# Performance work log

Measured on AMD Instinct MI355X. Metric: run time of the kernel, lower is better.

The kernel has to match this reference:

```python
import jax, jax.numpy as jnp
import numpy as np

B, C_IN, FH, TW = 64, 8, 128, 128
FBINS, A, M_ARR, M_SRC = 257, 360, 4, 2
EPS = 1e-6


def _conv2d(x, w):
    return jax.lax.conv_general_dilated(x, w, (1, 1), 'SAME', dimension_numbers=('NCHW', 'OIHW', 'NCHW'))


def _bn(x, g, b, m, v):
    sh = (1, -1, 1, 1)
    return (x - m.reshape(sh)) * jax.lax.rsqrt(v.reshape(sh) + 1e-5) * g.reshape(sh) + b.reshape(sh)


def _pool2(x):
    b_, c, h, w = x.shape
    return x.reshape(b_, c, h // 2, 2, w // 2, 2).max(axis=(3, 5))


def _block(x, w, g, b, m, v):
    return _pool2(jax.nn.relu(_bn(_conv2d(x, w), g, b, m, v)))


def _conv1d(x, w, b):
    return jax.lax.conv_general_dilated(x, w, (1,), 'SAME', dimension_numbers=('NCH', 'OIH', 'NCH')) + b[None, :, None]


def setup_inputs() -> dict:
    ks = jax.random.split(jax.random.key(0), 16)
    r = lambda i, shp, s=1.0: jax.random.normal(ks[i], shp, dtype=jnp.float32) * s
    d = {
        'X': r(0, (B, C_IN, FH, TW)),
        'sv_real': r(1, (B, FBINS, A, M_ARR)),
        'sv_imag': r(2, (B, FBINS, A, M_ARR)),
        'correlation': jnp.zeros((1,), jnp.float32),
        'conv1_w': r(3, (64, C_IN, 3, 3), 0.1),
        'conv2_w': r(4, (64, 64, 3, 3), 0.04),
        'conv3_w': r(5, (64, 64, 3, 3), 0.04),
        'conv4_w': r(6, (FBINS, 64, 3, 3), 0.04),
        'fc_w': r(7, (32, 64), 0.1),
        'fc_b': jnp.zeros((32,), jnp.float32),
        'convs2_w': r(8, (FBINS, FBINS, 3), 0.02),
        'convs2_b': jnp.zeros((FBINS,), jnp.float32),
        'convs1_w': r(9, (1, FBINS, 3), 0.03),
        'convs1_b': jnp.zeros((1,), jnp.float32),
        'ca_w1': r(10, (16, FBINS), 0.06),
        'ca_w2': r(11, (FBINS, 16), 0.2),
    }
    for i, c in [(1, 64), (2, 64), (3, 64), (4, FBINS)]:
        d[f'bn{i}_g'] = jnp.ones((c,), jnp.float32)
        d[f'bn{i}_b'] = jnp.zeros((c,), jnp.float32)
        d[f'bn{i}_m'] = jnp.zeros((c,), jnp.float32)
        d[f'bn{i}_v'] = jnp.ones((c,), jnp.float32)
    return d


def reference(X, sv_real, sv_imag, correlation,
              conv1_w, bn1_g, bn1_b, bn1_m, bn1_v,
              conv2_w, bn2_g, bn2_b, bn2_m, bn2_v,
              conv3_w, bn3_g, bn3_b, bn3_m, bn3_v,
              conv4_w, bn4_g, bn4_b, bn4_m, bn4_v,
              fc_w, fc_b, convs2_w, convs2_b, convs1_w, convs1_b,
              ca_w1, ca_w2):
    b_ = X.shape[0]
    # CNN encoder: (B,8,128,128) -> (B,257,8,8)
    z = _block(X, conv1_w, bn1_g, bn1_b, bn1_m, bn1_v)
    z = _block(z, conv2_w, bn2_g, bn2_b, bn2_m, bn2_v)
    z = _block(z, conv3_w, bn3_g, bn3_b, bn3_m, bn3_v)
    z = _block(z, conv4_w, bn4_g, bn4_b, bn4_m, bn4_v)
    z = z.reshape(b_, FBINS, -1) @ fc_w.T + fc_b            # (B,257,32)
    z = z.reshape(b_, FBINS, C_IN // 2, C_IN)               # (B,257,4,8)
    Rz = jax.lax.complex(z[..., :M_ARR], z[..., M_ARR:])    # (B,257,4,4)
    # hermitianize + diagonal loading
    Rz = 0.5 * (Rz + jnp.conj(jnp.swapaxes(Rz, -1, -2)))
    Rz = Rz + 1e-5 * jnp.eye(M_ARR, dtype=Rz.dtype)
    _, evecs = jnp.linalg.eigh(Rz)                          # ascending eigenvalues
    Un = evecs[..., ::-1][..., M_SRC:]                      # noise subspace (B,F,4,2)
    UnUnH = Un @ jnp.conj(jnp.swapaxes(Un, -1, -2))         # (B,F,4,4)
    svc = jnp.conj(jax.lax.complex(sv_real, sv_imag))       # (B,F,A,4)
    # faithful to torch code: denom[a] = sum_{m,n} conj(sv[a,m]) UnUnH[m,n] conj(sv[a,n])
    denom = jnp.real(jnp.einsum('bfam,bfmn,bfan->bfa', svc, UnUnH, svc))
    spectrum = 1.0 / jnp.maximum(denom, EPS)                # (B,257,360)
    spectrum = jax.nn.leaky_relu(_conv1d(spectrum, convs2_w, convs2_b), 0.1)
    # channel attention over the 257 freq channels
    y = spectrum.mean(-1)                                   # (B,257)
    att = jax.nn.sigmoid(jax.nn.relu(y @ ca_w1.T) @ ca_w2.T)
    spectrum = spectrum * att[:, :, None]
    spectrum = jax.nn.sigmoid(_conv1d(spectrum, convs1_w, convs1_b))[:, 0, :]  # (B,360)
    # soft-argmax over top-5 peaks
    angles = jnp.linspace(0.0, 360.0, A + 1)[:-1]
    vals, idx = jax.lax.top_k(spectrum, 5)
    wts = jax.nn.softmax(20.0 * vals, axis=-1)
    doa = (wts * angles[idx]).sum(-1)[:, None]              # (B,1)
    return doa, spectrum
```

## Files before the change

kernel.cpp:

```cpp
#include <hip/hip_runtime.h>

typedef unsigned short u16;
typedef unsigned int u32;
typedef short short8 __attribute__((ext_vector_type(8)));
typedef float f32x4 __attribute__((ext_vector_type(4)));

#define NB 64
#define NFB 257
#define NANG 360

template<int V> struct IC { static constexpr int value = V; };

__device__ __forceinline__ u16 f2bf(float x) {
    u32 u = __float_as_uint(x);
    u = (u + 0x7fffu + ((u >> 16) & 1u)) >> 16;
    return (u16)u;
}
__device__ __forceinline__ float bf2f(u16 h) { return __uint_as_float(((u32)h) << 16); }


__global__ __launch_bounds__(256) void bnprep(
    const float* g1, const float* b1, const float* m1, const float* v1,
    const float* g2, const float* b2, const float* m2, const float* v2,
    const float* g3, const float* b3, const float* m3, const float* v3,
    const float* g4, const float* b4, const float* m4, const float* v4,
    float* out)
{
    int L = blockIdx.x;
    const float* gs[4] = {g1, g2, g3, g4};
    const float* bs[4] = {b1, b2, b3, b4};
    const float* ms[4] = {m1, m2, m3, m4};
    const float* vs[4] = {v1, v2, v3, v4};
    int n = (L == 3) ? 257 : 64;
    float* sc = out + L * 1024;
    float* bi = sc + 512;
    for (int i = threadIdx.x; i < n; i += 256) {
        float s = gs[L][i] * rsqrtf(vs[L][i] + 1e-5f);
        sc[i] = s;
        bi[i] = bs[L][i] - ms[L][i] * s;
    }
}

__global__ __launch_bounds__(256) void bpack(
    const float* __restrict__ w, u16* __restrict__ Bp,
    int CREAL, int OCREAL, int NT, int KCC, int NFTOT)
{
    int i = blockIdx.x * 256 + threadIdx.x;
    int total = NT * KCC * 2 * NFTOT * 64;
    if (i >= total) return;
    int lane = i & 63;
    int t = i >> 6;
    int nf = t % NFTOT;
    int th = t / NFTOT;
    int h = th & 1;
    int chunk = th >> 1;
    int s = chunk / KCC, kc = chunk % KCC;
    int n = nf * 16 + (lane & 15);
    int k0 = kc * 32 + (lane >> 4) * 8;
    u16 o8[8];
    #pragma unroll
    for (int e = 0; e < 8; ++e) {
        int k = k0 + e;
        float v = 0.f;
        if (k < CREAL && n < OCREAL) v = w[((size_t)n * CREAL + k) * NT + s];
        u16 hh = f2bf(v);
        o8[e] = (h == 0) ? hh : f2bf(v - bf2f(hh));
    }
    u16* d = Bp + (size_t)i * 8;
    #pragma unroll
    for (int e = 0; e < 8; ++e) d[e] = o8[e];
}

__global__ __launch_bounds__(256) void bpack1(const float* __restrict__ w, u16* __restrict__ Bp)
{
    int i = blockIdx.x * 256 + threadIdx.x;
    if (i >= 3 * 2 * 4 * 64) return;
    int lane = i & 63;
    int t = i >> 6;
    int nf = t % 4;
    int th = t / 4;
    int h = th & 1;
    int ky = th >> 1;
    int n = nf * 16 + (lane & 15);
    int q = lane >> 4;
    u16 o8[8];
    #pragma unroll
    for (int e = 0; e < 8; ++e) {
        float v = (q < 3) ? w[((size_t)(n * 8 + e) * 3 + ky) * 3 + q] : 0.f;
        u16 hh = f2bf(v);
        o8[e] = (h == 0) ? hh : f2bf(v - bf2f(hh));
    }
    u16* d = Bp + (size_t)i * 8;
    #pragma unroll
    for (int e = 0; e < 8; ++e) d[e] = o8[e];
}

__global__ __launch_bounds__(256) void xpack_kernel(
    const float* __restrict__ X, u16* __restrict__ xp)
{
    __shared__ float Xs[8][132];
    int bid = blockIdx.x;
    int prow = bid % 130;
    int b = bid / 130;
    bool inr = (prow >= 1 && prow <= 128);
    for (int i = threadIdx.x; i < 8 * 130; i += 256) {
        int c = i / 130, pcol = i % 130;
        float v = 0.f;
        if (inr && pcol >= 1 && pcol <= 128)
            v = X[(((size_t)b * 8 + c) * 128 + (prow - 1)) * 128 + (pcol - 1)];
        Xs[c][pcol] = v;
    }
    __syncthreads();
    for (int p = threadIdx.x; p < 130; p += 256) {
        short8 h8, l8;
        #pragma unroll
        for (int c = 0; c < 8; ++c) {
            float f = Xs[c][p];
            u16 hh = f2bf(f);
            h8[c] = (short)hh;
            l8[c] = (short)f2bf(f - bf2f(hh));
        }
        size_t o = (((size_t)b * 130 + prow) * 130 + p) * 16;
        *(short8*)(xp + o) = h8;
        *(short8*)(xp + o + 8) = l8;
    }
}

__global__ __launch_bounds__(256) void zpad(
    u32* buf, int Bn, int Hp, int Wp, int wpp, int doCols)
{
    int perB = 2 * Wp + (doCols ? 2 * (Hp - 2) : 0);
    long total = (long)Bn * perB * wpp;
    for (long idx = blockIdx.x * 256L + threadIdx.x; idx < total; idx += (long)gridDim.x * 256) {
        int w = (int)(idx % wpp);
        long t = idx / wpp;
        int p = (int)(t % perB);
        int b = (int)(t / perB);
        int row, col;
        if (p < Wp) { row = 0; col = p; }
        else if (p < 2 * Wp) { row = Hp - 1; col = p - Wp; }
        else { int pp = p - 2 * Wp; row = 1 + (pp >> 1); col = (pp & 1) ? (Wp - 1) : 0; }
        buf[(((size_t)b * Hp + row) * Wp + col) * (size_t)wpp + w] = 0;
    }
}

__global__ __launch_bounds__(256) void conv_c1(
    const u16* __restrict__ A, const u16* __restrict__ Bp,
    const float* __restrict__ esc, const float* __restrict__ ebi,
    u16* __restrict__ O)
{
    constexpr int Wst = 130, Hp = 130;
    constexpr int SROWS = 5;
    constexpr int SPIX = SROWS * Wst;
    __shared__ __align__(16) char sm[SPIX * 48];

    int bid = blockIdx.x;
    int ytile = bid % 64;
    int b = bid / 64;
    int y0 = ytile * 2;
    int tid = threadIdx.x;
    int wv = tid >> 6;
    int l = tid & 63;
    int r = l & 15, q = l >> 4;

    #pragma unroll
    for (int it = 0; it < 3; ++it) {
        int pix = tid + it * 256;
        int prow = y0 + pix / Wst, pcol = pix % Wst;
        uint4 v0 = {0, 0, 0, 0}, v1 = {0, 0, 0, 0};
        if (pix < SPIX && prow < Hp) {
            const u16* src = A + (((size_t)b * Hp + prow) * Wst + pcol) * 16;
            v0 = *(const uint4*)src;
            v1 = *(const uint4*)(src + 8);
        }
        if (pix < SPIX) {
            *(uint4*)(sm + pix * 48) = v0;
            *(uint4*)(sm + pix * 48 + 16) = v1;
        }
    }
    __syncthreads();

    f32x4 acc[4][4] = {};

    #pragma unroll
    for (int ky = 0; ky < 3; ++ky) {
        short8 bh[4], bl[4];
        #pragma unroll
        for (int ni = 0; ni < 4; ++ni) {
            const u16* bt = Bp + ((size_t)(ky * 2) * 4 + ni) * 512 + l * 8;
            bh[ni] = *(const short8*)bt;
            bl[ni] = *(const short8*)(bt + 4 * 512);
        }
        short8 ah[4], al[4];
        #pragma unroll
        for (int mi = 0; mi < 4; ++mi) {
            int pf = wv * 2 + (mi >> 1);
            int y = mi & 1;
            int p = (y + ky) * Wst + pf * 16 + r + q;
            ah[mi] = *(const short8*)(sm + p * 48);
            al[mi] = *(const short8*)(sm + p * 48 + 16);
        }
        #pragma unroll
        for (int ni = 0; ni < 4; ++ni)
            #pragma unroll
            for (int mi = 0; mi < 4; ++mi)
                acc[mi][ni] = __builtin_amdgcn_mfma_f32_16x16x32_bf16(ah[mi], bh[ni], acc[mi][ni], 0, 0, 0);
        #pragma unroll
        for (int ni = 0; ni < 4; ++ni)
            #pragma unroll
            for (int mi = 0; mi < 4; ++mi)
                acc[mi][ni] = __builtin_amdgcn_mfma_f32_16x16x32_bf16(ah[mi], bl[ni], acc[mi][ni], 0, 0, 0);
        #pragma unroll
        for (int ni = 0; ni < 4; ++ni)
            #pragma unroll
            for (int mi = 0; mi < 4; ++mi)
                acc[mi][ni] = __builtin_amdgcn_mfma_f32_16x16x32_bf16(al[mi], bh[ni], acc[mi][ni], 0, 0, 0);
    }

    #pragma unroll
    for (int ni = 0; ni < 4; ++ni) {
        int oc = ni * 16 + r;
        float sc0 = esc[oc], bi0 = ebi[oc];
        #pragma unroll
        for (int pi = 0; pi < 2; ++pi) {
            int pf = wv * 2 + pi;
            #pragma unroll
            for (int k = 0; k < 2; ++k) {
                float m = -3.4e38f;
                #pragma unroll
                for (int dmi = 0; dmi < 2; ++dmi)
                    #pragma unroll
                    for (int dj = 0; dj < 2; ++dj)
                        m = fmaxf(m, fmaf(acc[2 * pi + dmi][ni][2 * k + dj], sc0, bi0));
                m = fmaxf(m, 0.f);
                int x2 = pf * 8 + q * 2 + k;
                size_t base = (((size_t)b * 66 + (y0 / 2 + 1)) * 66 + (x2 + 1)) * 128;
                u16* d = O + base + ((oc >> 5) << 6) + (oc & 31);
                u16 hh = f2bf(m);
                d[0] = hh;
                d[32] = f2bf(m - bf2f(hh));
            }
        }
    }
}

template<int H, int W, int OC, int R, int NF, int MFW, int OUTMODE, int NFTOT>
__global__ __launch_bounds__(256) void conv_gemm(
    const u16* __restrict__ A, const u16* __restrict__ Bp,
    const float* __restrict__ esc, const float* __restrict__ ebi,
    u16* __restrict__ O, float* __restrict__ Of)
{
    constexpr int Wst = W + 2, Hp = H + 2;
    constexpr int SROWS = R + 2;
    constexpr int SPIX = SROWS * Wst;
    constexpr int XF = W / 16;
    constexpr int HT = H / R;
    constexpr int GR = SPIX * 4;
    constexpr int ROUNDS = (GR + 255) / 256;
    __shared__ __align__(16) char sm[SPIX * 128];

    int bid = blockIdx.x;
    int ytile = bid % HT;
    int b = bid / HT;
    int tid = threadIdx.x;
    int wv = tid >> 6;
    int l = tid & 63;
    int r = l & 15, q = l >> 4;
    int y0 = ytile * R;
    int nfg0 = blockIdx.y * NF;

    f32x4 acc[MFW][NF] = {};
    short8 Bh[2][NF], Bl[2][NF];

    auto loadB = [&](int buf, int chunk) {
        #pragma unroll
        for (int ni = 0; ni < NF; ++ni) {
            const u16* bt = Bp + ((size_t)(chunk * 2) * NFTOT + nfg0 + ni) * 512 + l * 8;
            Bh[buf][ni] = *(const short8*)bt;
            Bl[buf][ni] = *(const short8*)(bt + (size_t)NFTOT * 512);
        }
    };

    #pragma unroll
    for (int it = 0; it < ROUNDS; ++it) {
        int idx = tid + it * 256;
        int pix = idx >> 2, sub = idx & 3;
        int prow = y0 + pix / Wst, pcol = pix % Wst;
        uint4 v0 = {0, 0, 0, 0}, v1 = {0, 0, 0, 0};
        if (idx < GR && prow < Hp) {
            const u16* src = A + (((size_t)b * Hp + prow) * Wst + pcol) * 128 + sub * 8;
            v0 = *(const uint4*)src;
            v1 = *(const uint4*)(src + 32);
        }
        if (idx < GR) {
            *(uint4*)(sm + pix * 128 + ((sub ^ (pix & 7)) << 4)) = v0;
            *(uint4*)(sm + pix * 128 + (((sub + 4) ^ (pix & 7)) << 4)) = v1;
        }
    }
    loadB(0, 0);
    __syncthreads();

    auto computePhase = [&](auto csc) {
        constexpr int cs = decltype(csc)::value;
        #pragma unroll
        for (int s = 0; s < 9; ++s) {
            int cur = (cs * 9 + s) & 1;
            if (s < 8) loadB(cur ^ 1, (s + 1) * 2 + cs);
            else if (cs == 0) loadB(cur ^ 1, 1);
            int ky = s / 3, kx = s % 3;
            short8 ah[MFW], al[MFW];
            #pragma unroll
            for (int mi = 0; mi < MFW; ++mi) {
                int pf = wv * (MFW / 2) + (mi >> 1);
                int y = (pf / XF) * 2 + (mi & 1);
                int xf = pf % XF;
                int p = (y + ky) * Wst + xf * 16 + kx + r;
                int off = p * 128 + ((q ^ (p & 7)) << 4);
                ah[mi] = *(const short8*)(sm + off);
                al[mi] = *(const short8*)(sm + (off ^ 64));
            }
            #pragma unroll
            for (int ni = 0; ni < NF; ++ni)
                #pragma unroll
                for (int mi = 0; mi < MFW; ++mi)
                    acc[mi][ni] = __builtin_amdgcn_mfma_f32_16x16x32_bf16(ah[mi], Bh[cur][ni], acc[mi][ni], 0, 0, 0);
            #pragma unroll
            for (int ni = 0; ni < NF; ++ni)
                #pragma unroll
                for (int mi = 0; mi < MFW; ++mi)
                    acc[mi][ni] = __builtin_amdgcn_mfma_f32_16x16x32_bf16(ah[mi], Bl[cur][ni], acc[mi][ni], 0, 0, 0);
            #pragma unroll
            for (int ni = 0; ni < NF; ++ni)
                #pragma unroll
                for (int mi = 0; mi < MFW; ++mi)
                    acc[mi][ni] = __builtin_amdgcn_mfma_f32_16x16x32_bf16(al[mi], Bh[cur][ni], acc[mi][ni], 0, 0, 0);
        }
    };

    uint4 r0[ROUNDS], r1[ROUNDS];
    #pragma unroll
    for (int it = 0; it < ROUNDS; ++it) {
        int idx = tid + it * 256;
        int pix = idx >> 2, sub = idx & 3;
        int prow = y0 + pix / Wst, pcol = pix % Wst;
        r0[it] = (uint4){0, 0, 0, 0};
        r1[it] = (uint4){0, 0, 0, 0};
        if (idx < GR && prow < Hp) {
            const u16* src = A + (((size_t)b * Hp + prow) * Wst + pcol) * 128 + 64 + sub * 8;
            r0[it] = *(const uint4*)src;
            r1[it] = *(const uint4*)(src + 32);
        }
    }
    computePhase(IC<0>{});
    __syncthreads();
    #pragma unroll
    for (int it = 0; it < ROUNDS; ++it) {
        int idx = tid + it * 256;
        int pix = idx >> 2, sub = idx & 3;
        if (idx < GR) {
            *(uint4*)(sm + pix * 128 + ((sub ^ (pix & 7)) << 4)) = r0[it];
            *(uint4*)(sm + pix * 128 + (((sub + 4) ^ (pix & 7)) << 4)) = r1[it];
        }
    }
    __syncthreads();
    computePhase(IC<1>{});

    #pragma unroll
    for (int ni = 0; ni < NF; ++ni) {
        int oc = (nfg0 + ni) * 16 + r;
        float sc0 = esc[oc], bi0 = ebi[oc];
        #pragma unroll
        for (int pi = 0; pi < MFW / 2; ++pi) {
            int pf = wv * (MFW / 2) + pi;
            int y2 = y0 / 2 + pf / XF;
            int xb = (pf % XF) * 8 + q * 2;
            #pragma unroll
            for (int k = 0; k < 2; ++k) {
                float m = -3.4e38f;
                #pragma unroll
                for (int dmi = 0; dmi < 2; ++dmi)
                    #pragma unroll
                    for (int dj = 0; dj < 2; ++dj)
                        m = fmaxf(m, fmaf(acc[2 * pi + dmi][ni][2 * k + dj], sc0, bi0));
                m = fmaxf(m, 0.f);
                int x2 = xb + k;
                if (OUTMODE == 0) {
                    size_t base = (((size_t)b * (H / 2 + 2) + y2 + 1) * (W / 2 + 2) + (x2 + 1)) * 128;
                    u16* d = O + base + ((oc >> 5) << 6) + (oc & 31);
                    u16 hh = f2bf(m);
                    d[0] = hh;
                    d[32] = f2bf(m - bf2f(hh));
                } else {
                    if (oc < OC)
                        Of[(((size_t)b * (H / 2) + y2) * (W / 2) + x2) * (size_t)OC + oc] = m;
                }
            }
        }
    }
}

__global__ __launch_bounds__(256) void convs2_gemm(
    const u16* __restrict__ A, const u16* __restrict__ Bp,
    const float* __restrict__ bia, float* __restrict__ sp2,
    float* __restrict__ part)
{
    constexpr int SPIX = 194;
    constexpr int GR = SPIX * 4;
    constexpr int ROUNDS = 4;
    __shared__ __align__(16) char sm[SPIX * 128];

    int bid = blockIdx.x;
    int tt = bid & 1;
    int b = bid >> 1;
    int nt = blockIdx.y;
    int t0 = tt * 192;
    int tid = threadIdx.x;
    int wv = tid >> 6;
    int l = tid & 63;
    int r = l & 15, q = l >> 4;

    f32x4 acc[3][3] = {};
    short8 Bh[2][3], Bl[2][3];

    auto loadB = [&](int buf, int chunk) {
        #pragma unroll
        for (int ni = 0; ni < 3; ++ni) {
            const u16* bt = Bp + ((size_t)(chunk * 2) * 18 + nt * 3 + ni) * 512 + l * 8;
            Bh[buf][ni] = *(const short8*)bt;
            Bl[buf][ni] = *(const short8*)(bt + 18 * 512);
        }
    };
    uint4 g0[ROUNDS], g1[ROUNDS];

    auto stageIssue = [&](int cs) {
        #pragma unroll
        for (int it = 0; it < ROUNDS; ++it) {
            int idx = tid + it * 256;
            int pix = idx >> 2, sub = idx & 3;
            int gp = t0 + pix;
            g0[it] = (uint4){0, 0, 0, 0};
            g1[it] = (uint4){0, 0, 0, 0};
            if (idx < GR && gp < 362) {
                const u16* src = A + ((size_t)b * 362 + gp) * 576 + cs * 64 + sub * 8;
                g0[it] = *(const uint4*)src;
                g1[it] = *(const uint4*)(src + 32);
            }
        }
    };
    auto stageWrite = [&]() {
        #pragma unroll
        for (int it = 0; it < ROUNDS; ++it) {
            int idx = tid + it * 256;
            int pix = idx >> 2, sub = idx & 3;
            if (idx < GR) {
                *(uint4*)(sm + pix * 128 + ((sub ^ (pix & 7)) << 4)) = g0[it];
                *(uint4*)(sm + pix * 128 + (((sub + 4) ^ (pix & 7)) << 4)) = g1[it];
            }
        }
    };

    stageIssue(0);
    stageWrite();
    loadB(0, 0);
    __syncthreads();

    #pragma unroll
    for (int cs = 0; cs < 9; ++cs) {
        if (cs < 8) stageIssue(cs + 1);
        #pragma unroll
        for (int ky = 0; ky < 3; ++ky) {
            int cur = (cs * 3 + ky) & 1;
            if (ky < 2) loadB(cur ^ 1, (ky + 1) * 9 + cs);
            else if (cs < 8) loadB(cur ^ 1, cs + 1);
            #pragma unroll
            for (int mi = 0; mi < 3; ++mi) {
                int p = (wv * 3 + mi) * 16 + r + ky;
                int off = p * 128 + ((q ^ (p & 7)) << 4);
                short8 ah = *(const short8*)(sm + off);
                short8 al = *(const short8*)(sm + (off ^ 64));
                #pragma unroll
                for (int ni = 0; ni < 3; ++ni)
                    acc[mi][ni] = __builtin_amdgcn_mfma_f32_16x16x32_bf16(ah, Bh[cur][ni], acc[mi][ni], 0, 0, 0);
                #pragma unroll
                for (int ni = 0; ni < 3; ++ni)
                    acc[mi][ni] = __builtin_amdgcn_mfma_f32_16x16x32_bf16(ah, Bl[cur][ni], acc[mi][ni], 0, 0, 0);
                #pragma unroll
                for (int ni = 0; ni < 3; ++ni)
                    acc[mi][ni] = __builtin_amdgcn_mfma_f32_16x16x32_bf16(al, Bh[cur][ni], acc[mi][ni], 0, 0, 0);
            }
        }
        __syncthreads();
        if (cs < 8) {
            stageWrite();
            __syncthreads();
        }
    }

    float psum[3] = {0.f, 0.f, 0.f};
    #pragma unroll
    for (int ni = 0; ni < 3; ++ni) {
        int n = (nt * 3 + ni) * 16 + r;
        if (n >= NFB) continue;
        float bi0 = bia[n];
        #pragma unroll
        for (int mi = 0; mi < 3; ++mi) {
            int tb = t0 + (wv * 3 + mi) * 16 + q * 4;
            #pragma unroll
            for (int j = 0; j < 4; ++j) {
                int t = tb + j;
                if (t < NANG) {
                    float v = acc[mi][ni][j] + bi0;
                    v = (v >= 0.f) ? v : 0.1f * v;
                    sp2[((size_t)b * NANG + t) * NFB + n] = v;
                    psum[ni] += v;
                }
            }
        }
    }
    float* wred = (float*)sm;
    #pragma unroll
    for (int ni = 0; ni < 3; ++ni) {
        float s = psum[ni];
        s += __shfl_down(s, 32, 64);
        s += __shfl_down(s, 16, 64);
        if (q == 0) wred[(wv * 3 + ni) * 16 + r] = s;
    }
    __syncthreads();
    if (tid < 48) {
        int ni = tid / 16, rr = tid % 16;
        float tot = wred[(0 * 3 + ni) * 16 + rr] + wred[(1 * 3 + ni) * 16 + rr]
                  + wred[(2 * 3 + ni) * 16 + rr] + wred[(3 * 3 + ni) * 16 + rr];
        int n = (nt * 3 + ni) * 16 + rr;
        if (n < NFB) part[((size_t)b * 2 + tt) * NFB + n] = tot;
    }
}

__global__ __launch_bounds__(256) void fc_kernel(
    const float* __restrict__ z, const float* __restrict__ fw,
    const float* __restrict__ fb, float* __restrict__ zfc)
{
    int bid = blockIdx.x;
    int ftile = bid % 33;
    int b = bid / 33;
    int j = threadIdx.x & 31;
    int f = ftile * 8 + (threadIdx.x >> 5);
    if (f >= 257) return;
    const float* zb = z + (size_t)b * 16448;
    float a = fb[j];
    #pragma unroll 8
    for (int s = 0; s < 64; ++s) a = fmaf(zb[s * 257 + f], fw[j * 64 + s], a);
    zfc[((size_t)b * 257 + f) * 32 + j] = a;
}

__global__ __launch_bounds__(64) void eigh_kernel(const float* __restrict__ z, double* __restrict__ rp)
{
    int idx = blockIdx.x * 64 + threadIdx.x;
    if (idx >= NB * NFB) return;
    const float* zr = z + (size_t)idx * 32;
    double Ar[4][4], Ai[4][4], Vr[4][4], Vi[4][4];
    #pragma unroll
    for (int m = 0; m < 4; ++m)
        #pragma unroll
        for (int n = 0; n < 4; ++n) {
            Ar[m][n] = 0.5 * ((double)zr[m * 8 + n] + (double)zr[n * 8 + m]);
            Ai[m][n] = 0.5 * ((double)zr[m * 8 + n + 4] - (double)zr[n * 8 + m + 4]);
            Vr[m][n] = (m == n) ? 1.0 : 0.0;
            Vi[m][n] = 0.0;
        }
    #pragma unroll
    for (int m = 0; m < 4; ++m) Ar[m][m] += 1e-5;

    for (int sweep = 0; sweep < 8; ++sweep) {
        #pragma unroll
        for (int p = 0; p < 3; ++p)
            #pragma unroll
            for (int qq = p + 1; qq < 4; ++qq) {
                double apr = Ar[p][qq], api = Ai[p][qq];
                double rmod = sqrt(apr * apr + api * api);
                if (rmod < 1e-300) continue;
                double cph = apr / rmod, sph = api / rmod;
                double tau = (Ar[qq][qq] - Ar[p][p]) / (2.0 * rmod);
                double t = (tau >= 0.0) ? (-1.0 / (tau + sqrt(1.0 + tau * tau)))
                                        : (1.0 / (-tau + sqrt(1.0 + tau * tau)));
                double c = 1.0 / sqrt(1.0 + t * t);
                double s = t * c;
                double wr = s * cph, wi = s * sph;
                #pragma unroll
                for (int i = 0; i < 4; ++i) {
                    double xr = Ar[i][p], xi = Ai[i][p];
                    double yr = Ar[i][qq], yi = Ai[i][qq];
                    Ar[i][p] = c * xr + (wr * yr + wi * yi);
                    Ai[i][p] = c * xi + (wr * yi - wi * yr);
                    Ar[i][qq] = c * yr - (wr * xr - wi * xi);
                    Ai[i][qq] = c * yi - (wr * xi + wi * xr);
                }
                #pragma unroll
                for (int i = 0; i < 4; ++i) {
                    double xr = Ar[p][i], xi = Ai[p][i];
                    double yr = Ar[qq][i], yi = Ai[qq][i];
                    Ar[p][i] = c * xr + (wr * yr - wi * yi);
                    Ai[p][i] = c * xi + (wr * yi + wi * yr);
                    Ar[qq][i] = c * yr - (wr * xr + wi * xi);
                    Ai[qq][i] = c * yi - (wr * xi - wi * xr);
                }
                #pragma unroll
                for (int i = 0; i < 4; ++i) {
                    double xr = Vr[i][p], xi = Vi[i][p];
                    double yr = Vr[i][qq], yi = Vi[i][qq];
                    Vr[i][p] = c * xr + (wr * yr + wi * yi);
                    Vi[i][p] = c * xi + (wr * yi - wi * yr);
                    Vr[i][qq] = c * yr - (wr * xr - wi * xi);
                    Vi[i][qq] = c * yi - (wr * xi + wi * xr);
                }
            }
    }
    double ev[4] = {Ar[0][0], Ar[1][1], Ar[2][2], Ar[3][3]};
    int i0 = 0;
    #pragma unroll
    for (int k = 1; k < 4; ++k) if (ev[k] < ev[i0]) i0 = k;
    int i1 = (i0 == 0) ? 1 : 0;
    #pragma unroll
    for (int k = 0; k < 4; ++k) if (k != i0 && ev[k] < ev[i1]) i1 = k;
    double* o = rp + (size_t)idx * 16;
    #pragma unroll
    for (int m = 0; m < 4; ++m)
        #pragma unroll
        for (int n = 0; n < 4; ++n)
            o[m * 4 + n] = Vr[m][i0] * Vr[n][i0] + Vi[m][i0] * Vi[n][i0]
                         + Vr[m][i1] * Vr[n][i1] + Vi[m][i1] * Vi[n][i1];
}

__global__ __launch_bounds__(256) void music_kernel(
    const float4* __restrict__ svr, const float4* __restrict__ svi,
    const double* __restrict__ rp, u16* __restrict__ mu)
{
    __shared__ double P[32][16];
    __shared__ float T[32][33];
    int bid = blockIdx.x;
    int at = bid % 12; bid /= 12;
    int ft = bid % 9;
    int b = bid / 9;
    int f0 = ft * 32, a0 = at * 32;
    int tid = threadIdx.x;
    for (int i = tid; i < 32 * 16; i += 256) {
        int fi = i >> 4, j = i & 15;
        int f = f0 + fi;
        P[fi][j] = (f < 257) ? rp[((size_t)b * 257 + f) * 16 + j] : 0.0;
    }
    __syncthreads();
    int asub = tid & 31, fsub = tid >> 5;
    int a = a0 + asub;
    #pragma unroll
    for (int k2 = 0; k2 < 4; ++k2) {
        int fl = fsub + 8 * k2;
        int f = f0 + fl;
        float val = 0.f;
        if (a < 360 && f < 257) {
            float4 u = svr[((size_t)b * 257 + f) * 360 + a];
            float4 w = svi[((size_t)b * 257 + f) * 360 + a];
            const double* Pf = P[fl];
            double ua[4] = {u.x, u.y, u.z, u.w};
            double wa[4] = {w.x, w.y, w.z, w.w};
            double qa = 0.0, qb = 0.0;
            #pragma unroll
            for (int m = 0; m < 4; ++m)
                #pragma unroll
                for (int n = 0; n < 4; ++n) {
                    double pmn = Pf[m * 4 + n];
                    qa += pmn * ua[m] * ua[n];
                    qb += pmn * wa[m] * wa[n];
                }
            double den = qa - qb;
            val = (float)(1.0 / fmax(den, 1e-6));
        }
        T[asub][fl] = val;
    }
    __syncthreads();
    int sec0 = f0 >> 5;
    #pragma unroll
    for (int p = 0; p < 4; ++p) {
        int row = p * 8 + (tid >> 5);
        int fc = tid & 31;
        int a2 = a0 + row;
        if (a2 < 360) {
            float v = T[row][fc];
            u16* d = mu + ((size_t)b * 362 + a2 + 1) * 576 + (size_t)sec0 * 64 + fc;
            u16 hh = f2bf(v);
            d[0] = hh;
            d[32] = f2bf(v - bf2f(hh));
        }
    }
}

__global__ __launch_bounds__(256) void attn_finish(
    const float* __restrict__ part, const float* __restrict__ w1,
    const float* __restrict__ w2, float* __restrict__ att)
{
    __shared__ float ys[257];
    __shared__ float hs[16];
    int b = blockIdx.x;
    int tid = threadIdx.x;
    for (int f = tid; f < 257; f += 256) {
        float s = part[((size_t)b * 2 + 0) * 257 + f] + part[((size_t)b * 2 + 1) * 257 + f];
        ys[f] = s * (1.0f / 360.0f);
    }
    __syncthreads();
    if (tid < 16) {
        float h = 0.f;
        for (int c = 0; c < 257; ++c) h = fmaf(ys[c], w1[(size_t)tid * 257 + c], h);
        hs[tid] = fmaxf(h, 0.f);
    }
    __syncthreads();
    for (int o = tid; o < 257; o += 256) {
        float a = 0.f;
        #pragma unroll
        for (int j = 0; j < 16; ++j) a = fmaf(hs[j], w2[(size_t)o * 16 + j], a);
        att[(size_t)b * 257 + o] = 1.0f / (1.0f + expf(-a));
    }
}

__global__ __launch_bounds__(256) void convs1_kernel(
    const float* __restrict__ sp2, const float* __restrict__ att,
    const float* __restrict__ w, const float* __restrict__ bb,
    float* __restrict__ outS)
{
    int bid = blockIdx.x;
    int tt = bid % 90;
    int b = bid / 90;
    int wv = threadIdx.x >> 6, l = threadIdx.x & 63;
    int t = tt * 4 + wv;
    float s = 0.f;
    for (int f = l; f < 257; f += 64) {
        float av = att[(size_t)b * 257 + f];
        float w0 = w[f * 3] * av, w1 = w[f * 3 + 1] * av, w2 = w[f * 3 + 2] * av;
        const float* col = sp2 + (size_t)b * 360 * 257 + f;
        if (t > 0)   s = fmaf(w0, col[(size_t)(t - 1) * 257], s);
        s = fmaf(w1, col[(size_t)t * 257], s);
        if (t < 359) s = fmaf(w2, col[(size_t)(t + 1) * 257], s);
    }
    #pragma unroll
    for (int off = 32; off > 0; off >>= 1) s += __shfl_down(s, off, 64);
    if (l == 0) outS[(size_t)b * 360 + t] = 1.0f / (1.0f + expf(-(s + bb[0])));
}

__global__ __launch_bounds__(64) void doa_kernel(const float* __restrict__ spec, float* __restrict__ doa)
{
    int b = blockIdx.x;
    int l = threadIdx.x;
    const float* s = spec + (size_t)b * NANG;
    float v[6];
    #pragma unroll
    for (int j = 0; j < 6; ++j) {
        int idx = l + 64 * j;
        v[j] = (idx < NANG) ? s[idx] : -3.4e38f;
    }
    float wvv[5]; int wii[5];
    #pragma unroll
    for (int k = 0; k < 5; ++k) {
        float bv = v[0]; int bj = 0;
        #pragma unroll
        for (int j = 1; j < 6; ++j)
            if (v[j] > bv) { bv = v[j]; bj = j; }
        int bi = l + 64 * bj;
        #pragma unroll
        for (int off = 1; off < 64; off <<= 1) {
            float ov = __shfl_xor(bv, off, 64);
            int oi = __shfl_xor(bi, off, 64);
            if (ov > bv || (ov == bv && oi < bi)) { bv = ov; bi = oi; }
        }
        wvv[k] = bv; wii[k] = bi;
        if ((bi & 63) == l) {
            int j = bi >> 6;
            #pragma unroll
            for (int jj = 0; jj < 6; ++jj)
                if (jj == j) v[jj] = -3.4e38f;
        }
    }
    if (l == 0) {
        float m = wvv[0];
        float wsum = 0.f, asum = 0.f;
        #pragma unroll
        for (int k = 0; k < 5; ++k) {
            float e = expf(20.0f * (wvv[k] - m));
            wsum += e;
            asum += e * (float)wii[k];
        }
        doa[b] = asum / wsum;
    }
}

extern "C" void kernel_launch(void* const* d_in, const int* in_sizes, int n_in,
                              void* d_out, int out_size, void* d_ws, size_t ws_size,
                              hipStream_t stream)
{
    const float* X    = (const float*)d_in[0];
    const float* svr  = (const float*)d_in[1];
    const float* svi  = (const float*)d_in[2];
    const float* c1w  = (const float*)d_in[4];
    const float* c2w  = (const float*)d_in[5];
    const float* c3w  = (const float*)d_in[6];
    const float* c4w  = (const float*)d_in[7];
    const float* fcw  = (const float*)d_in[8];
    const float* fcb  = (const float*)d_in[9];
    const float* s2w  = (const float*)d_in[10];
    const float* s2b  = (const float*)d_in[11];
    const float* s1w  = (const float*)d_in[12];
    const float* s1b  = (const float*)d_in[13];
    const float* caw1 = (const float*)d_in[14];
    const float* caw2 = (const float*)d_in[15];
    const float* bn1g = (const float*)d_in[16]; const float* bn1b = (const float*)d_in[17];
    const float* bn1m = (const float*)d_in[18]; const float* bn1v = (const float*)d_in[19];
    const float* bn2g = (const float*)d_in[20]; const float* bn2b = (const float*)d_in[21];
    const float* bn2m = (const float*)d_in[22]; const float* bn2v = (const float*)d_in[23];
    const float* bn3g = (const float*)d_in[24]; const float* bn3b = (const float*)d_in[25];
    const float* bn3m = (const float*)d_in[26]; const float* bn3v = (const float*)d_in[27];
    const float* bn4g = (const float*)d_in[28]; const float* bn4b = (const float*)d_in[29];
    const float* bn4m = (const float*)d_in[30]; const float* bn4v = (const float*)d_in[31];

    char* wsb = (char*)d_ws;
    u16* xp = (u16*)(wsb + 0);
    u16* c3 = (u16*)(wsb + 0);
    u16* mu = (u16*)(wsb + 0);
    const size_t Bb = 34611200;
    u16*   c2  = (u16*)(wsb + Bb);
    float*  zbuf = (float*)(wsb + Bb);
    float*  zfc  = (float*)(wsb + Bb + 4210688);
    double* rp   = (double*)(wsb + Bb + 6316032);
    float*  sp2  = (float*)(wsb + Bb + 8421376);
    float*  part = (float*)(wsb + Bb + 32106496);
    float*  att  = (float*)(wsb + Bb + 32501248);
    const size_t Cb = Bb + 71368704;
    u16* c4  = (u16*)(wsb + Cb);
    u16* bp1 = (u16*)(wsb + Cb + 5308416);
    u16* bp2 = (u16*)(wsb + Cb + 5382144);
    u16* bp3 = (u16*)(wsb + Cb + 5529600);
    u16* bp4 = (u16*)(wsb + Cb + 5677056);
    u16* bp5 = (u16*)(wsb + Cb + 6414336);
    float* bns = (float*)(wsb + Cb + 7409664);

    float* outD = (float*)d_out;
    float* outS = (float*)d_out + 64;

    bnprep<<<4, 256, 0, stream>>>(bn1g, bn1b, bn1m, bn1v, bn2g, bn2b, bn2m, bn2v,
                                  bn3g, bn3b, bn3m, bn3v, bn4g, bn4b, bn4m, bn4v, bns);
    bpack1<<<6, 256, 0, stream>>>(c1w, bp1);
    bpack<<<36, 256, 0, stream>>>(c2w, bp2, 64, 64, 9, 2, 4);
    bpack<<<36, 256, 0, stream>>>(c3w, bp3, 64, 64, 9, 2, 4);
    bpack<<<180, 256, 0, stream>>>(c4w, bp4, 64, 257, 9, 2, 20);
    bpack<<<243, 256, 0, stream>>>(s2w, bp5, 257, 257, 3, 9, 18);
    xpack_kernel<<<64 * 130, 256, 0, stream>>>(X, xp);
    zpad<<<4160, 256, 0, stream>>>((u32*)c2, 64, 66, 66, 64, 1);
    zpad<<<1088, 256, 0, stream>>>((u32*)c4, 64, 18, 18, 64, 1);

    conv_c1<<<64 * 64, 256, 0, stream>>>(xp, bp1, bns, bns + 512, c2);
    zpad<<<2112, 256, 0, stream>>>((u32*)c3, 64, 34, 34, 64, 1);
    conv_gemm<64, 64, 64, 2, 4, 2, 0, 4>
        <<<dim3(64 * 32, 1), 256, 0, stream>>>(c2, bp2, bns + 1024, bns + 1536, c3, nullptr);
    conv_gemm<32, 32, 64, 4, 4, 2, 0, 4>
        <<<dim3(64 * 8, 1), 256, 0, stream>>>(c3, bp3, bns + 2048, bns + 2560, c4, nullptr);
    zpad<<<144, 256, 0, stream>>>((u32*)mu, 64, 362, 1, 288, 0);
    conv_gemm<16, 16, 257, 8, 4, 2, 1, 20>
        <<<dim3(64 * 2, 5), 256, 0, stream>>>(c4, bp4, bns + 3072, bns + 3584, nullptr, zbuf);

    fc_kernel<<<64 * 33, 256, 0, stream>>>(zbuf, fcw, fcb, zfc);
    eigh_kernel<<<NFB, 64, 0, stream>>>(zfc, rp);
    music_kernel<<<64 * 108, 256, 0, stream>>>((const float4*)svr, (const float4*)svi, rp, mu);
    convs2_gemm<<<dim3(64 * 2, 6), 256, 0, stream>>>(mu, bp5, s2b, sp2, part);

    attn_finish<<<64, 256, 0, stream>>>(part, caw1, caw2, att);
    convs1_kernel<<<64 * 90, 256, 0, stream>>>(sp2, att, s1w, s1b, outS);
    doa_kernel<<<64, 64, 0, stream>>>(outS, outD);
}
```

Before: 416.5 us.

## Merge prep kernels, drop register prefetch staging, retile convs2 into three tiles

Fuses the BN prep, the five weight-pack kernels and the input packer into one prep_kernel, and merges two zero-pad launches into one, to cut launch count. Conv_gemm and convs2_gemm drop their register-held prefetch of the next channel slice and instead load straight to shared memory after a barrier. This lowers register pressure but stops overlapping global loads with MFMA work. Convs2 now splits the 360 angles into three 128-wide tiles instead of two 192-wide ones, which raises block count and shrinks the per-wave accumulators. The attention partial-sum reduction is updated to read three partials.

Result: faster. 395.0 us (-5.2%).

```diff
diff --git a/kernel.cpp b/kernel.cpp
--- a/kernel.cpp
+++ b/kernel.cpp
@@ -19,33 +19,10 @@
 __device__ __forceinline__ float bf2f(u16 h) { return __uint_as_float(((u32)h) << 16); }
 
 
-__global__ __launch_bounds__(256) void bnprep(
-    const float* g1, const float* b1, const float* m1, const float* v1,
-    const float* g2, const float* b2, const float* m2, const float* v2,
-    const float* g3, const float* b3, const float* m3, const float* v3,
-    const float* g4, const float* b4, const float* m4, const float* v4,
-    float* out)
-{
-    int L = blockIdx.x;
-    const float* gs[4] = {g1, g2, g3, g4};
-    const float* bs[4] = {b1, b2, b3, b4};
-    const float* ms[4] = {m1, m2, m3, m4};
-    const float* vs[4] = {v1, v2, v3, v4};
-    int n = (L == 3) ? 257 : 64;
-    float* sc = out + L * 1024;
-    float* bi = sc + 512;
-    for (int i = threadIdx.x; i < n; i += 256) {
-        float s = gs[L][i] * rsqrtf(vs[L][i] + 1e-5f);
-        sc[i] = s;
-        bi[i] = bs[L][i] - ms[L][i] * s;
-    }
-}
-
-__global__ __launch_bounds__(256) void bpack(
+__device__ __forceinline__ void bpack_body(
     const float* __restrict__ w, u16* __restrict__ Bp,
-    int CREAL, int OCREAL, int NT, int KCC, int NFTOT)
-{
-    int i = blockIdx.x * 256 + threadIdx.x;
+    int CREAL, int OCREAL, int NT, int KCC, int NFTOT, int i)
+{
     int total = NT * KCC * 2 * NFTOT * 64;
     if (i >= total) return;
     int lane = i & 63;
@@ -71,59 +48,107 @@
     for (int e = 0; e < 8; ++e) d[e] = o8[e];
 }
 
-__global__ __launch_bounds__(256) void bpack1(const float* __restrict__ w, u16* __restrict__ Bp)
-{
-    int i = blockIdx.x * 256 + threadIdx.x;
-    if (i >= 3 * 2 * 4 * 64) return;
-    int lane = i & 63;
-    int t = i >> 6;
-    int nf = t % 4;
-    int th = t / 4;
-    int h = th & 1;
-    int ky = th >> 1;
-    int n = nf * 16 + (lane & 15);
-    int q = lane >> 4;
-    u16 o8[8];
-    #pragma unroll
-    for (int e = 0; e < 8; ++e) {
-        float v = (q < 3) ? w[((size_t)(n * 8 + e) * 3 + ky) * 3 + q] : 0.f;
-        u16 hh = f2bf(v);
-        o8[e] = (h == 0) ? hh : f2bf(v - bf2f(hh));
-    }
-    u16* d = Bp + (size_t)i * 8;
-    #pragma unroll
-    for (int e = 0; e < 8; ++e) d[e] = o8[e];
-}
-
-__global__ __launch_bounds__(256) void xpack_kernel(
-    const float* __restrict__ X, u16* __restrict__ xp)
+__global__ __launch_bounds__(256) void prep_kernel(
+    const float* __restrict__ X, u16* __restrict__ xp,
+    const float* __restrict__ c1w, u16* __restrict__ bp1,
+    const float* __restrict__ c2w, u16* __restrict__ bp2,
+    const float* __restrict__ c3w, u16* __restrict__ bp3,
+    const float* __restrict__ c4w, u16* __restrict__ bp4,
+    const float* __restrict__ s2w, u16* __restrict__ bp5,
+    const float* g1, const float* b1, const float* m1, const float* v1,
+    const float* g2, const float* b2, const float* m2, const float* v2,
+    const float* g3, const float* b3, const float* m3, const float* v3,
+    const float* g4, const float* b4, const float* m4, const float* v4,
+    float* __restrict__ bns)
 {
     __shared__ float Xs[8][132];
-    int bid = blockIdx.x;
-    int prow = bid % 130;
-    int b = bid / 130;
-    bool inr = (prow >= 1 && prow <= 128);
-    for (int i = threadIdx.x; i < 8 * 130; i += 256) {
-        int c = i / 130, pcol = i % 130;
-        float v = 0.f;
-        if (inr && pcol >= 1 && pcol <= 128)
-            v = X[(((size_t)b * 8 + c) * 128 + (prow - 1)) * 128 + (pcol - 1)];
-        Xs[c][pcol] = v;
-    }
-    __syncthreads();
-    for (int p = threadIdx.x; p < 130; p += 256) {
-        short8 h8, l8;
-        #pragma unroll
-        for (int c = 0; c < 8; ++c) {
-            float f = Xs[c][p];
-            u16 hh = f2bf(f);
-            h8[c] = (short)hh;
-            l8[c] = (short)f2bf(f - bf2f(hh));
-        }
-        size_t o = (((size_t)b * 130 + prow) * 130 + p) * 16;
-        *(short8*)(xp + o) = h8;
-        *(short8*)(xp + o + 8) = l8;
-    }
+    int blk = blockIdx.x;
+    int tid = threadIdx.x;
+    if (blk < 4) {
+        int L = blk;
+        const float* gs[4] = {g1, g2, g3, g4};
+        const float* bs[4] = {b1, b2, b3, b4};
+        const float* ms[4] = {m1, m2, m3, m4};
+        const float* vs[4] = {v1, v2, v3, v4};
+        int n = (L == 3) ? 257 : 64;
+        float* sc = bns + L * 1024;
+        float* bi = sc + 512;
+        for (int i = tid; i < n; i += 256) {
+            float s = gs[L][i] * rsqrtf(vs[L][i] + 1e-5f);
+            sc[i] = s;
+            bi[i] = bs[L][i] - ms[L][i] * s;
+        }
+    } else if (blk < 10) {
+        int i = (blk - 4) * 256 + tid;
+        if (i < 3 * 2 * 4 * 64) {
+            int lane = i & 63;
+            int t = i >> 6;
+            int nf = t % 4;
+            int th = t / 4;
+            int h = th & 1;
+            int ky = th >> 1;
+            int n = nf * 16 + (lane & 15);
+            int q = lane >> 4;
+            u16 o8[8];
+            #pragma unroll
+            for (int e = 0; e < 8; ++e) {
+                float v = (q < 3) ? c1w[((size_t)(n * 8 + e) * 3 + ky) * 3 + q] : 0.f;
+                u16 hh = f2bf(v);
+                o8[e] = (h == 0) ? hh : f2bf(v - bf2f(hh));
+            }
+            u16* d = bp1 + (size_t)i * 8;
+            #pragma unroll
+            for (int e = 0; e < 8; ++e) d[e] = o8[e];
+        }
+    } else if (blk < 46) {
+        bpack_body(c2w, bp2, 64, 64, 9, 2, 4, (blk - 10) * 256 + tid);
+    } else if (blk < 82) {
+        bpack_body(c3w, bp3, 64, 64, 9, 2, 4, (blk - 46) * 256 + tid);
+    } else if (blk < 262) {
+        bpack_body(c4w, bp4, 64, 257, 9, 2, 20, (blk - 82) * 256 + tid);
+    } else if (blk < 505) {
+        bpack_body(s2w, bp5, 257, 257, 3, 9, 18, (blk - 262) * 256 + tid);
+    } else {
+        int row = blk - 505;
+        int prow = row % 130;
+        int b = row / 130;
+        bool inr = (prow >= 1 && prow <= 128);
+        for (int i = tid; i < 8 * 130; i += 256) {
+            int c = i / 130, pcol = i % 130;
+            float v = 0.f;
+            if (inr && pcol >= 1 && pcol <= 128)
+                v = X[(((size_t)b * 8 + c) * 128 + (prow - 1)) * 128 + (pcol - 1)];
+            Xs[c][pcol] = v;
+        }
+        __syncthreads();
+        for (int p = tid; p < 130; p += 256) {
+            short8 h8, l8;
+            #pragma unroll
+            for (int c = 0; c < 8; ++c) {
+                float f = Xs[c][p];
+                u16 hh = f2bf(f);
+                h8[c] = (short)hh;
+                l8[c] = (short)f2bf(f - bf2f(hh));
+            }
+            size_t o = (((size_t)b * 130 + prow) * 130 + p) * 16;
+            *(short8*)(xp + o) = h8;
+            *(short8*)(xp + o + 8) = l8;
+        }
+    }
+}
+
+__device__ __forceinline__ void zpad_body(u32* buf, int Hp, int Wp, int wpp, int doCols, long idx)
+{
+    int perB = 2 * Wp + (doCols ? 2 * (Hp - 2) : 0);
+    int w = (int)(idx % wpp);
+    long t = idx / wpp;
+    int p = (int)(t % perB);
+    int b = (int)(t / perB);
+    int row, col;
+    if (p < Wp) { row = 0; col = p; }
+    else if (p < 2 * Wp) { row = Hp - 1; col = p - Wp; }
+    else { int pp = p - 2 * Wp; row = 1 + (pp >> 1); col = (pp & 1) ? (Wp - 1) : 0; }
+    buf[(((size_t)b * Hp + row) * Wp + col) * (size_t)wpp + w] = 0;
 }
 
 __global__ __launch_bounds__(256) void zpad(
@@ -131,16 +156,17 @@
 {
     int perB = 2 * Wp + (doCols ? 2 * (Hp - 2) : 0);
     long total = (long)Bn * perB * wpp;
-    for (long idx = blockIdx.x * 256L + threadIdx.x; idx < total; idx += (long)gridDim.x * 256) {
-        int w = (int)(idx % wpp);
-        long t = idx / wpp;
-        int p = (int)(t % perB);
-        int b = (int)(t / perB);
-        int row, col;
-        if (p < Wp) { row = 0; col = p; }
-        else if (p < 2 * Wp) { row = Hp - 1; col = p - Wp; }
-        else { int pp = p - 2 * Wp; row = 1 + (pp >> 1); col = (pp & 1) ? (Wp - 1) : 0; }
-        buf[(((size_t)b * Hp + row) * Wp + col) * (size_t)wpp + w] = 0;
+    for (long idx = blockIdx.x * 256L + threadIdx.x; idx < total; idx += (long)gridDim.x * 256)
+        zpad_body(buf, Hp, Wp, wpp, doCols, idx);
+}
+
+__global__ __launch_bounds__(256) void zpad_init(u32* c2b, u32* c4b)
+{
+    const long T1 = 64L * 260 * 64;
+    const long T2 = 64L * 68 * 64;
+    for (long idx = blockIdx.x * 256L + threadIdx.x; idx < T1 + T2; idx += (long)gridDim.x * 256) {
+        if (idx < T1) zpad_body(c2b, 66, 66, 64, 1, idx);
+        else          zpad_body(c4b, 18, 18, 64, 1, idx - T1);
     }
 }
 
@@ -281,24 +307,24 @@
         }
     };
 
-    #pragma unroll
-    for (int it = 0; it < ROUNDS; ++it) {
-        int idx = tid + it * 256;
-        int pix = idx >> 2, sub = idx & 3;
-        int prow = y0 + pix / Wst, pcol = pix % Wst;
-        uint4 v0 = {0, 0, 0, 0}, v1 = {0, 0, 0, 0};
-        if (idx < GR && prow < Hp) {
-            const u16* src = A + (((size_t)b * Hp + prow) * Wst + pcol) * 128 + sub * 8;
-            v0 = *(const uint4*)src;
-            v1 = *(const uint4*)(src + 32);
-        }
-        if (idx < GR) {
-            *(uint4*)(sm + pix * 128 + ((sub ^ (pix & 7)) << 4)) = v0;
-            *(uint4*)(sm + pix * 128 + (((sub + 4) ^ (pix & 7)) << 4)) = v1;
-        }
-    }
-    loadB(0, 0);
-    __syncthreads();
+    auto stage = [&](int cs) {
+        #pragma unroll
+        for (int it = 0; it < ROUNDS; ++it) {
+            int idx = tid + it * 256;
+            int pix = idx >> 2, sub = idx & 3;
+            int prow = y0 + pix / Wst, pcol = pix % Wst;
+            uint4 v0 = {0, 0, 0, 0}, v1 = {0, 0, 0, 0};
+            if (idx < GR && prow < Hp) {
+                const u16* src = A + (((size_t)b * Hp + prow) * Wst + pcol) * 128 + cs * 64 + sub * 8;
+                v0 = *(const uint4*)src;
+                v1 = *(const uint4*)(src + 32);
+            }
+            if (idx < GR) {
+                *(uint4*)(sm + pix * 128 + ((sub ^ (pix & 7)) << 4)) = v0;
+                *(uint4*)(sm + pix * 128 + (((sub + 4) ^ (pix & 7)) << 4)) = v1;
+            }
+        }
+    };
 
     auto computePhase = [&](auto csc) {
         constexpr int cs = decltype(csc)::value;
@@ -337,31 +363,12 @@
         }
     };
 
-    uint4 r0[ROUNDS], r1[ROUNDS];
-    #pragma unroll
-    for (int it = 0; it < ROUNDS; ++it) {
-        int idx = tid + it * 256;
-        int pix = idx >> 2, sub = idx & 3;
-        int prow = y0 + pix / Wst, pcol = pix % Wst;
-        r0[it] = (uint4){0, 0, 0, 0};
-        r1[it] = (uint4){0, 0, 0, 0};
-        if (idx < GR && prow < Hp) {
-            const u16* src = A + (((size_t)b * Hp + prow) * Wst + pcol) * 128 + 64 + sub * 8;
-            r0[it] = *(const uint4*)src;
-            r1[it] = *(const uint4*)(src + 32);
-        }
-    }
+    stage(0);
+    loadB(0, 0);
+    __syncthreads();
     computePhase(IC<0>{});
     __syncthreads();
-    #pragma unroll
-    for (int it = 0; it < ROUNDS; ++it) {
-        int idx = tid + it * 256;
-        int pix = idx >> 2, sub = idx & 3;
-        if (idx < GR) {
-            *(uint4*)(sm + pix * 128 + ((sub ^ (pix & 7)) << 4)) = r0[it];
-            *(uint4*)(sm + pix * 128 + (((sub + 4) ^ (pix & 7)) << 4)) = r1[it];
-        }
-    }
+    stage(1);
     __syncthreads();
     computePhase(IC<1>{});
 
@@ -404,22 +411,21 @@
     const float* __restrict__ bia, float* __restrict__ sp2,
     float* __restrict__ part)
 {
-    constexpr int SPIX = 194;
+    constexpr int SPIX = 130;
     constexpr int GR = SPIX * 4;
-    constexpr int ROUNDS = 4;
     __shared__ __align__(16) char sm[SPIX * 128];
 
     int bid = blockIdx.x;
-    int tt = bid & 1;
-    int b = bid >> 1;
+    int tt = bid % 3;
+    int b = bid / 3;
     int nt = blockIdx.y;
-    int t0 = tt * 192;
+    int t0 = tt * 128;
     int tid = threadIdx.x;
     int wv = tid >> 6;
     int l = tid & 63;
     int r = l & 15, q = l >> 4;
 
-    f32x4 acc[3][3] = {};
+    f32x4 acc[2][3] = {};
     short8 Bh[2][3], Bl[2][3];
 
     auto loadB = [&](int buf, int chunk) {
@@ -430,68 +436,64 @@
             Bl[buf][ni] = *(const short8*)(bt + 18 * 512);
         }
     };
-    uint4 g0[ROUNDS], g1[ROUNDS];
-
-    auto stageIssue = [&](int cs) {
-        #pragma unroll
-        for (int it = 0; it < ROUNDS; ++it) {
+
+    auto stage = [&](int cs) {
+        #pragma unroll
+        for (int it = 0; it < 3; ++it) {
             int idx = tid + it * 256;
             int pix = idx >> 2, sub = idx & 3;
             int gp = t0 + pix;
-            g0[it] = (uint4){0, 0, 0, 0};
-            g1[it] = (uint4){0, 0, 0, 0};
+            uint4 v0 = {0, 0, 0, 0}, v1 = {0, 0, 0, 0};
             if (idx < GR && gp < 362) {
                 const u16* src = A + ((size_t)b * 362 + gp) * 576 + cs * 64 + sub * 8;
-                g0[it] = *(const uint4*)src;
-                g1[it] = *(const uint4*)(src + 32);
+                v0 = *(const uint4*)src;
+                v1 = *(const uint4*)(src + 32);
+            }
+            if (idx < GR) {
+                *(uint4*)(sm + pix * 128 + ((sub ^ (pix & 7)) << 4)) = v0;
+                *(uint4*)(sm + pix * 128 + (((sub + 4) ^ (pix & 7)) << 4)) = v1;
             }
         }
     };
-    auto stageWrite = [&]() {
-        #pragma unroll
-        for (int it = 0; it < ROUNDS; ++it) {
-            int idx = tid + it * 256;
-            int pix = idx >> 2, sub = idx & 3;
-            if (idx < GR) {
-                *(uint4*)(sm + pix * 128 + ((sub ^ (pix & 7)) << 4)) = g0[it];
-                *(uint4*)(sm + pix * 128 + (((sub + 4) ^ (pix & 7)) << 4)) = g1[it];
-            }
-        }
-    };
-
-    stageIssue(0);
-    stageWrite();
+
+    stage(0);
     loadB(0, 0);
     __syncthreads();
 
     #pragma unroll
     for (int cs = 0; cs < 9; ++cs) {
-        if (cs < 8) stageIssue(cs + 1);
         #pragma unroll
         for (int ky = 0; ky < 3; ++ky) {
             int cur = (cs * 3 + ky) & 1;
             if (ky < 2) loadB(cur ^ 1, (ky + 1) * 9 + cs);
             else if (cs < 8) loadB(cur ^ 1, cs + 1);
-            #pragma unroll
-            for (int mi = 0; mi < 3; ++mi) {
-                int p = (wv * 3 + mi) * 16 + r + ky;
+            short8 ah[2], al[2];
+            #pragma unroll
+            for (int mi = 0; mi < 2; ++mi) {
+                int p = (wv * 2 + mi) * 16 + r + ky;
                 int off = p * 128 + ((q ^ (p & 7)) << 4);
-                short8 ah = *(const short8*)(sm + off);
-                short8 al = *(const short8*)(sm + (off ^ 64));
-                #pragma unroll
-                for (int ni = 0; ni < 3; ++ni)
-                    acc[mi][ni] = __builtin_amdgcn_mfma_f32_16x16x32_bf16(ah, Bh[cur][ni], acc[mi][ni], 0, 0, 0);
-                #pragma unroll
-                for (int ni = 0; ni < 3; ++ni)
-                    acc[mi][ni] = __builtin_amdgcn_mfma_f32_16x16x32_bf16(ah, Bl[cur][ni], acc[mi][ni], 0, 0, 0);
-                #pragma unroll
-                for (int ni = 0; ni < 3; ++ni)
-                    acc[mi][ni] = __builtin_amdgcn_mfma_f32_16x16x32_bf16(al, Bh[cur][ni], acc[mi][ni], 0, 0, 0);
-            }
+                ah[mi] = *(const short8*)(sm + off);
+                al[mi] = *(const short8*)(sm + (off ^ 64));
+            }
+            #pragma unroll
+            for (int ni = 0; ni < 3; ++ni)
+                #pragma unroll
+                for (int mi = 0; mi < 2; ++mi)
+                    acc[mi][ni] = __builtin_amdgcn_mfma_f32_16x16x32_bf16(ah[mi], Bh[cur][ni], acc[mi][ni], 0, 0, 0);
+            #pragma unroll
+            for (int ni = 0; ni < 3; ++ni)
+                #pragma unroll
+                for (int mi = 0; mi < 2; ++mi)
+                    acc[mi][ni] = __builtin_amdgcn_mfma_f32_16x16x32_bf16(ah[mi], Bl[cur][ni], acc[mi][ni], 0, 0, 0);
+            #pragma unroll
+            for (int ni = 0; ni < 3; ++ni)
+                #pragma unroll
+                for (int mi = 0; mi < 2; ++mi)
+                    acc[mi][ni] = __builtin_amdgcn_mfma_f32_16x16x32_bf16(al[mi], Bh[cur][ni], acc[mi][ni], 0, 0, 0);
         }
         __syncthreads();
         if (cs < 8) {
-            stageWrite();
+            stage(cs + 1);
             __syncthreads();
         }
     }
@@ -503,8 +505,8 @@
         if (n >= NFB) continue;
         float bi0 = bia[n];
         #pragma unroll
-        for (int mi = 0; mi < 3; ++mi) {
-            int tb = t0 + (wv * 3 + mi) * 16 + q * 4;
+        for (int mi = 0; mi < 2; ++mi) {
+            int tb = t0 + (wv * 2 + mi) * 16 + q * 4;
             #pragma unroll
             for (int j = 0; j < 4; ++j) {
                 int t = tb + j;
@@ -531,7 +533,7 @@
         float tot = wred[(0 * 3 + ni) * 16 + rr] + wred[(1 * 3 + ni) * 16 + rr]
                   + wred[(2 * 3 + ni) * 16 + rr] + wred[(3 * 3 + ni) * 16 + rr];
         int n = (nt * 3 + ni) * 16 + rr;
-        if (n < NFB) part[((size_t)b * 2 + tt) * NFB + n] = tot;
+        if (n < NFB) part[((size_t)b * 3 + tt) * NFB + n] = tot;
     }
 }
 
@@ -701,7 +703,9 @@
     int b = blockIdx.x;
     int tid = threadIdx.x;
     for (int f = tid; f < 257; f += 256) {
-        float s = part[((size_t)b * 2 + 0) * 257 + f] + part[((size_t)b * 2 + 1) * 257 + f];
+        float s = part[((size_t)b * 3 + 0) * 257 + f]
+                + part[((size_t)b * 3 + 1) * 257 + f]
+                + part[((size_t)b * 3 + 2) * 257 + f];
         ys[f] = s * (1.0f / 360.0f);
     }
     __syncthreads();
@@ -841,16 +845,11 @@
     float* outD = (float*)d_out;
     float* outS = (float*)d_out + 64;
 
-    bnprep<<<4, 256, 0, stream>>>(bn1g, bn1b, bn1m, bn1v, bn2g, bn2b, bn2m, bn2v,
-                                  bn3g, bn3b, bn3m, bn3v, bn4g, bn4b, bn4m, bn4v, bns);
-    bpack1<<<6, 256, 0, stream>>>(c1w, bp1);
-    bpack<<<36, 256, 0, stream>>>(c2w, bp2, 64, 64, 9, 2, 4);
-    bpack<<<36, 256, 0, stream>>>(c3w, bp3, 64, 64, 9, 2, 4);
-    bpack<<<180, 256, 0, stream>>>(c4w, bp4, 64, 257, 9, 2, 20);
-    bpack<<<243, 256, 0, stream>>>(s2w, bp5, 257, 257, 3, 9, 18);
-    xpack_kernel<<<64 * 130, 256, 0, stream>>>(X, xp);
-    zpad<<<4160, 256, 0, stream>>>((u32*)c2, 64, 66, 66, 64, 1);
-    zpad<<<1088, 256, 0, stream>>>((u32*)c4, 64, 18, 18, 64, 1);
+    prep_kernel<<<8825, 256, 0, stream>>>(
+        X, xp, c1w, bp1, c2w, bp2, c3w, bp3, c4w, bp4, s2w, bp5,
+        bn1g, bn1b, bn1m, bn1v, bn2g, bn2b, bn2m, bn2v,
+        bn3g, bn3b, bn3m, bn3v, bn4g, bn4b, bn4m, bn4v, bns);
+    zpad_init<<<2048, 256, 0, stream>>>((u32*)c2, (u32*)c4);
 
     conv_c1<<<64 * 64, 256, 0, stream>>>(xp, bp1, bns, bns + 512, c2);
     zpad<<<2112, 256, 0, stream>>>((u32*)c3, 64, 34, 34, 64, 1);
@@ -865,7 +864,7 @@
     fc_kernel<<<64 * 33, 256, 0, stream>>>(zbuf, fcw, fcb, zfc);
     eigh_kernel<<<NFB, 64, 0, stream>>>(zfc, rp);
     music_kernel<<<64 * 108, 256, 0, stream>>>((const float4*)svr, (const float4*)svi, rp, mu);
-    convs2_gemm<<<dim3(64 * 2, 6), 256, 0, stream>>>(mu, bp5, s2b, sp2, part);
+    convs2_gemm<<<dim3(64 * 3, 6), 256, 0, stream>>>(mu, bp5, s2b, sp2, part);
 
     attn_finish<<<64, 256, 0, stream>>>(part, caw1, caw2, att);
     convs1_kernel<<<64 * 90, 256, 0, stream>>>(sp2, att, s1w, s1b, outS);
```
